# Performance work log

Hardware: AMD Instinct MI355X
Metric: run time of the kernel (lower is better)

## Reference

```python
import jax, jax.numpy as jnp
import numpy as np

ALPHA = 0.2
NEG_INF = -9e15


def setup_inputs() -> dict:
    key = jax.random.key(0)
    k1, k2, k3, k4 = jax.random.split(key, 4)
    B, N, C_IN, C_OUT, R, H = 8, 1024, 256, 256, 4, 4
    node_feats = jax.random.normal(k1, (B, N, C_IN), dtype=jnp.float32)
    adj_matrix = jax.random.randint(k2, (B, N, N, R), 0, 2, dtype=jnp.int32)
    # xavier_uniform with gain=1.414 for Linear(c_in, c_out) weights
    lim_w = 1.414 * np.sqrt(6.0 / (C_IN + C_OUT))
    W = jax.random.uniform(k3, (R, C_IN, C_OUT), minval=-lim_w, maxval=lim_w, dtype=jnp.float32)
    c_per = C_OUT // H
    lim_a = 1.414 * np.sqrt(6.0 / (H + 2 * c_per))
    a = jax.random.uniform(k4, (R, H, 2 * c_per), minval=-lim_a, maxval=lim_a, dtype=jnp.float32)
    return {"node_feats": node_feats, "adj_matrix": adj_matrix, "W": W, "a": a}


def reference(node_feats, adj_matrix, W, a):
    B, N, _ = node_feats.shape
    R, H = a.shape[0], a.shape[1]
    C = a.shape[2] // 2  # per-head feature dim
    out = jnp.zeros((B, N, H, C), dtype=node_feats.dtype)
    for r in range(R):
        # per-relation projection: [B,N,H,C]
        f = jnp.einsum('bnc,cd->bnd', node_feats, W[r]).reshape(B, N, H, C)
        a_l, a_r = a[r, :, :C], a[r, :, C:]
        # attention logit decomposes: a . [f_i || f_j] = a_l . f_i + a_r . f_j
        li = jnp.einsum('bnhc,hc->bnh', f, a_l)  # source-node term
        lj = jnp.einsum('bnhc,hc->bnh', f, a_r)  # target-node term
        logits = jax.nn.leaky_relu(li[:, :, None, :] + lj[:, None, :, :], ALPHA)  # [B,N,N,H]
        mask = adj_matrix[..., r] != 0  # [B,N,N]
        logits = jnp.where(mask[..., None], logits, NEG_INF)
        probs = jax.nn.softmax(logits, axis=2)
        out = out + jnp.einsum('bijh,bjhc->bihc', probs, f)
    # concat_heads=True
    return out.reshape(B, N, H * C)
```

## Files before the change

kernel.cpp:

```cpp
#include <hip/hip_runtime.h>
#include <math.h>

#define Bsz 8
#define Nn 1024
#define CIN 256
#define COUT 256
#define NR 4
#define NH 4

typedef unsigned short u16;
typedef __attribute__((ext_vector_type(8))) short bf16x8;
typedef __attribute__((ext_vector_type(4))) float f32x4;

#define OFF_LIP (16u << 20)
#define OFF_LJP ((16u << 20) + (512u << 10))
#define OFF_ADJM (17u << 20)
#define OFF_XBF (21u << 20)
#define OFF_WBFT (25u << 20)
#define OFF_WAL ((25u << 20) + (512u << 10))
#define OFF_WAR ((25u << 20) + (528u << 10))

#define LOG2E 1.4426950408889634f

__device__ __forceinline__ short f2bf(float x) {
  union { float f; unsigned u; } v; v.f = x;
  unsigned r = (v.u + 0x7FFFu + ((v.u >> 16) & 1u)) >> 16;
  return (short)r;
}

__device__ __forceinline__ float fast_exp2(float x) {
#if __has_builtin(__builtin_amdgcn_exp2f)
  return __builtin_amdgcn_exp2f(x);
#else
  return exp2f(x);
#endif
}

__device__ __forceinline__ void gl_lds16(const void* g, void* l) {
  __builtin_amdgcn_global_load_lds(
      (const __attribute__((address_space(1))) unsigned int*)(unsigned long long)g,
      (__attribute__((address_space(3))) unsigned int*)(unsigned int)(unsigned long long)l,
      16, 0, 0);
}

__global__ __launch_bounds__(256, 8)
void gatt_pack(const int4* __restrict__ adj4, unsigned long long* __restrict__ adjm) {
  const int t = threadIdx.x;
  const int wid = blockIdx.x * 4 + (t >> 6);
  const int lane = t & 63;
  const int jw = wid & 15;
  const int i = (wid >> 4) & 1023;
  const int b = wid >> 14;
  const int j = jw * 64 + lane;
  const int4 av = adj4[(size_t)(b * Nn + i) * Nn + j];
  const unsigned long long b0 = __ballot(av.x != 0);
  const unsigned long long b1 = __ballot(av.y != 0);
  const unsigned long long b2 = __ballot(av.z != 0);
  const unsigned long long b3 = __ballot(av.w != 0);
  if (lane < 4) {
    unsigned long long v = (lane == 0) ? b0 : (lane == 1) ? b1 : (lane == 2) ? b2 : b3;
    adjm[((size_t)((b * Nn + i) * NR + lane)) * 16 + jw] = v;
  }
}

__global__ __launch_bounds__(256, 8)
void gatt_xconv(const float4* __restrict__ X4, int4* __restrict__ Xbf4) {
  const int idx = blockIdx.x * 256 + threadIdx.x;
  const float4 a = X4[idx * 2], b = X4[idx * 2 + 1];
  u16 pk[8];
  pk[0] = (u16)f2bf(a.x); pk[1] = (u16)f2bf(a.y); pk[2] = (u16)f2bf(a.z); pk[3] = (u16)f2bf(a.w);
  pk[4] = (u16)f2bf(b.x); pk[5] = (u16)f2bf(b.y); pk[6] = (u16)f2bf(b.z); pk[7] = (u16)f2bf(b.w);
  Xbf4[idx] = *(int4*)pk;
}

__global__ __launch_bounds__(256, 4)
void gatt_wtrans(const float* __restrict__ W, u16* __restrict__ WbfT) {
  const int t = threadIdx.x;
  const int r = blockIdx.x >> 3, kc = blockIdx.x & 7;
  u16 pk[32];
#pragma unroll 8
  for (int kk = 0; kk < 32; ++kk)
    pk[kk] = (u16)f2bf(W[(size_t)r * 65536 + (size_t)(kc * 32 + kk) * COUT + t]);
  u16* dst = WbfT + (size_t)r * 65536 + (size_t)t * CIN + kc * 32;
#pragma unroll
  for (int q = 0; q < 4; ++q) *(int4*)(dst + q * 8) = *(int4*)(pk + q * 8);
}

__global__ __launch_bounds__(256, 4)
void gatt_wa(const float* __restrict__ W, const float* __restrict__ a,
             float* __restrict__ wa_l, float* __restrict__ wa_r) {
  const int t = threadIdx.x;
  const int r = blockIdx.x >> 2, h = blockIdx.x & 3;
  float sl = 0.f, sr = 0.f;
  const float* Wp = W + (size_t)r * 65536 + (size_t)t * COUT + h * 64;
  const float* ap = a + r * 512 + h * 128;
#pragma unroll 8
  for (int c = 0; c < 64; ++c) {
    const float wv = Wp[c];
    sl = fmaf(wv, ap[c], sl);
    sr = fmaf(wv, ap[64 + c], sr);
  }
  wa_l[(size_t)blockIdx.x * CIN + t] = sl;
  wa_r[(size_t)blockIdx.x * CIN + t] = sr;
}

__global__ __launch_bounds__(256, 4)
void gatt_logit(const float* __restrict__ X, const float4* __restrict__ wal4,
                const float4* __restrict__ war4, float* __restrict__ Lip,
                float* __restrict__ Ljp) {
  __shared__ float Xs[16 * 260];
  const int t = threadIdx.x;
  const int row0 = blockIdx.x * 16;
  {
    const int il = t >> 4, kq = t & 15;
    const float4* xp = (const float4*)(X + (size_t)(row0 + il) * CIN + kq * 16);
    float4* dst = (float4*)(Xs + il * 260 + kq * 16);
#pragma unroll
    for (int u = 0; u < 4; ++u) dst[u] = xp[u];
  }
  __syncthreads();
  const int rl = t >> 4, combo = t & 15;
  float li = 0.f, lj = 0.f;
#pragma unroll 8
  for (int k4 = 0; k4 < 64; ++k4) {
    const float4 x4 = *(const float4*)(Xs + rl * 260 + k4 * 4);
    const float4 wl = wal4[combo * 64 + k4];
    const float4 wr = war4[combo * 64 + k4];
    li += x4.x * wl.x + x4.y * wl.y + x4.z * wl.z + x4.w * wl.w;
    lj += x4.x * wr.x + x4.y * wr.y + x4.z * wr.z + x4.w * wr.w;
  }
  const int g = row0 + rl, b = g >> 10, n = g & 1023;
  const size_t idx = ((size_t)(combo * Bsz + b)) * Nn + n;
  Lip[idx] = li * LOG2E;
  Ljp[idx] = lj * LOG2E;
}

__global__ __launch_bounds__(256)
void gatt_fgemm(const u16* __restrict__ Xbf, const u16* __restrict__ WbfT,
                u16* __restrict__ fTf) {
  __shared__ u16 lds_w[8192];
  __shared__ u16 lds_x[2048];
  const int t = threadIdx.x;
  const int r = blockIdx.x & 3, b = (blockIdx.x >> 2) & 7, ntl = blockIdx.x >> 5;
  const int n0 = ntl * 64;
  const int g0 = b * Nn + n0;
  const int lane = t & 63, w = t >> 6;
  const int m = lane & 15, quad = lane >> 4;
  const int cw = w * 64;
  const int xq = quad ^ (m & 3);

  const u16* Wsrc = WbfT + (size_t)r * 65536;
  f32x4 acc[4][4];
#pragma unroll
  for (int ct = 0; ct < 4; ++ct)
#pragma unroll
    for (int nt = 0; nt < 4; ++nt) acc[ct][nt] = (f32x4){0.f, 0.f, 0.f, 0.f};

  for (int kc = 0; kc < 8; ++kc) {
    __syncthreads();
#pragma unroll
    for (int q = 0; q < 4; ++q) {
      const int s = q * 256 + t;
      const int c = s >> 2, ks = (s & 3) ^ (c & 3);
      gl_lds16(Wsrc + (size_t)c * CIN + kc * 32 + ks * 8, lds_w + s * 8);
    }
    {
      const int s = t;
      const int n = s >> 2, ks = (s & 3) ^ (n & 3);
      gl_lds16(Xbf + (size_t)(g0 + n) * CIN + kc * 32 + ks * 8, lds_x + s * 8);
    }
    __syncthreads();

    bf16x8 af[4], bfr[4];
#pragma unroll
    for (int ct = 0; ct < 4; ++ct)
      af[ct] = *(const bf16x8*)(lds_w + (cw + ct * 16 + m) * 32 + xq * 8);
#pragma unroll
    for (int nt = 0; nt < 4; ++nt)
      bfr[nt] = *(const bf16x8*)(lds_x + (nt * 16 + m) * 32 + xq * 8);
#pragma unroll
    for (int ct = 0; ct < 4; ++ct)
#pragma unroll
      for (int nt = 0; nt < 4; ++nt)
        acc[ct][nt] = __builtin_amdgcn_mfma_f32_16x16x32_bf16(af[ct], bfr[nt], acc[ct][nt], 0, 0, 0);
  }

  u16* fragbase = fTf + (size_t)(((r * Bsz + b) * 4 + w) * 128) * 512;
#pragma unroll
  for (int ct = 0; ct < 4; ++ct) {
#pragma unroll
    for (int ntf = 0; ntf < 4; ++ntf) {
      const int j = n0 + ntf * 16 + m;
      const int jb = j >> 5;
      const int qt = ((ntf & 1) << 1) | (m >> 3);
      const int e = m & 7;
      u16* dst = fragbase + (size_t)((jb * 4 + ct) * 512) + (qt * 16 + quad * 4) * 8 + e;
#pragma unroll
      for (int p = 0; p < 4; ++p) dst[p * 8] = (u16)f2bf(acc[ct][ntf][p]);
    }
  }
}

__global__ __launch_bounds__(256, 4)
void gatt_attn(const unsigned long long* __restrict__ adjm,
               const u16* __restrict__ fTf, const float* __restrict__ Lip,
               const float* __restrict__ Ljp, float* __restrict__ out) {
  __shared__ float ljs[4 * 1024];

  const int t = threadIdx.x;
  const int comb = blockIdx.x & 31;
  const int b = comb >> 2, r = comb & 3;
  const int i0 = (blockIdx.x >> 5) * 32;
  const int h = t >> 6, lane = t & 63;
  const int m = lane & 15, quad = lane >> 4;
  const int qo = quad * 8;

  {
#pragma unroll
    for (int q = 0; q < 4; ++q) {
      const int s = q * 256 + t;
      const int hh = s >> 8, off = s & 255;
      ((float4*)ljs)[hh * 256 + off] =
          ((const float4*)(Ljp + ((size_t)((r * NH + hh) * Bsz + b)) * Nn))[off];
    }
  }
  __syncthreads();

  const float* lipb = Lip + ((size_t)((r * NH + h) * Bsz + b)) * Nn;
  const float li0 = lipb[i0 + m];
  const float li1 = lipb[i0 + 16 + m];
  const unsigned long long* amp0 = adjm + ((size_t)((b * Nn + i0 + m) * NR + r)) * 16;
  const unsigned long long* amp1 = adjm + ((size_t)((b * Nn + i0 + 16 + m) * NR + r)) * 16;
  const bf16x8* fp = (const bf16x8*)fTf + (size_t)(((r * Bsz + b) * 4 + h)) * 8192;
  const float* ljh = ljs + h * Nn;

  bf16x8 ones;
#pragma unroll
  for (int e = 0; e < 8; ++e) ones[e] = (short)0x3F80;

  f32x4 acc[2][4], den[2];
#pragma unroll
  for (int iw = 0; iw < 2; ++iw) {
    den[iw] = (f32x4){0.f, 0.f, 0.f, 0.f};
#pragma unroll
    for (int nt = 0; nt < 4; ++nt) acc[iw][nt] = (f32x4){0.f, 0.f, 0.f, 0.f};
  }

  for (int jq = 0; jq < 16; ++jq) {
    const uint2 mw0 = *(const uint2*)(amp0 + jq);
    const uint2 mw1 = *(const uint2*)(amp1 + jq);
#pragma unroll
    for (int half = 0; half < 2; ++half) {
      const int jb = jq * 2 + half;
      const unsigned mb0 = ((half ? mw0.y : mw0.x) >> qo) & 0xFFu;
      const unsigned mb1 = ((half ? mw1.y : mw1.x) >> qo) & 0xFFu;
      const float4 la = *(const float4*)(ljh + jb * 32 + qo);
      const float4 lb = *(const float4*)(ljh + jb * 32 + qo + 4);
      const float ljv[8] = {la.x, la.y, la.z, la.w, lb.x, lb.y, lb.z, lb.w};
      bf16x8 bfr[4];
#pragma unroll
      for (int nt = 0; nt < 4; ++nt) bfr[nt] = fp[(jb * 4 + nt) * 64 + lane];
#pragma unroll
      for (int iw = 0; iw < 2; ++iw) {
        const float liv = iw ? li1 : li0;
        const unsigned mb = iw ? mb1 : mb0;
        unsigned wm[8];
#pragma unroll
        for (int e = 0; e < 8; ++e) {
          const float s = liv + ljv[e];
          const float ls = fmaxf(s, 0.2f * s);
          const float wv = fast_exp2(ls);
          const int msk = ((int)(mb << (31 - e))) >> 31;
          wm[e] = __float_as_uint(wv) & (unsigned)msk;
        }
        union { unsigned u[4]; bf16x8 v; } af;
#pragma unroll
        for (int k = 0; k < 4; ++k)
          af.u[k] = (wm[2 * k] >> 16) | (wm[2 * k + 1] & 0xFFFF0000u);
        den[iw] = __builtin_amdgcn_mfma_f32_16x16x32_bf16(af.v, ones, den[iw], 0, 0, 0);
#pragma unroll
        for (int nt = 0; nt < 4; ++nt)
          acc[iw][nt] = __builtin_amdgcn_mfma_f32_16x16x32_bf16(af.v, bfr[nt], acc[iw][nt], 0, 0, 0);
      }
    }
  }

#pragma unroll
  for (int iw = 0; iw < 2; ++iw) {
#pragma unroll
    for (int p = 0; p < 4; ++p) {
      const float inv = __builtin_amdgcn_rcpf(den[iw][p]);
      const int i = i0 + iw * 16 + quad * 4 + p;
      float* op = out + ((size_t)(b * Nn) + i) * COUT + h * 64 + m;
#pragma unroll
      for (int nt = 0; nt < 4; ++nt) atomicAdd(op + nt * 16, acc[iw][nt][p] * inv);
    }
  }
}

extern "C" void kernel_launch(void* const* d_in, const int* in_sizes, int n_in,
                              void* d_out, int out_size, void* d_ws, size_t ws_size,
                              hipStream_t stream) {
  const float* X = (const float*)d_in[0];
  const int4* adj4 = (const int4*)d_in[1];
  const float* W = (const float*)d_in[2];
  const float* a = (const float*)d_in[3];
  float* out = (float*)d_out;

  char* ws = (char*)d_ws;
  u16* fTf = (u16*)ws;
  float* Lip = (float*)(ws + OFF_LIP);
  float* Ljp = (float*)(ws + OFF_LJP);
  unsigned long long* adjm = (unsigned long long*)(ws + OFF_ADJM);
  u16* Xbf = (u16*)(ws + OFF_XBF);
  u16* WbfT = (u16*)(ws + OFF_WBFT);
  float* wa_l = (float*)(ws + OFF_WAL);
  float* wa_r = (float*)(ws + OFF_WAR);

  hipMemsetAsync(d_out, 0, (size_t)out_size * sizeof(float), stream);
  gatt_pack<<<dim3(32768), dim3(256), 0, stream>>>(adj4, adjm);
  gatt_xconv<<<dim3(1024), dim3(256), 0, stream>>>((const float4*)X, (int4*)Xbf);
  gatt_wtrans<<<dim3(32), dim3(256), 0, stream>>>(W, WbfT);
  gatt_wa<<<dim3(16), dim3(256), 0, stream>>>(W, a, wa_l, wa_r);
  gatt_logit<<<dim3(512), dim3(256), 0, stream>>>(X, (const float4*)wa_l,
                                                  (const float4*)wa_r, Lip, Ljp);
  gatt_fgemm<<<dim3(512), dim3(256), 0, stream>>>(Xbf, WbfT, fTf);
  gatt_attn<<<dim3(1024), dim3(256), 0, stream>>>(adjm, fTf, Lip, Ljp, out);
}
```

Measured before the change: 309.0 us.

## Merge prep kernels, fuse X conversion into logits, replace atomics with reduce

Merges the W transpose and W·a kernels into one launch, and converts X to bf16 inside the logit kernel so the separate conversion kernel goes away. The attention kernel now writes per-relation partial outputs to workspace with plain stores, and a new reduce kernel sums the four relations. This replaces the memset and the float atomics. The attention inner loop also switches to packed float2 math, sbfe mask extraction and perm-based bf16 packing to cut ALU work. In exchange it adds a 32 MB workspace round-trip for the partial outputs.

```diff
diff --git a/kernel.cpp b/kernel.cpp
--- a/kernel.cpp
+++ b/kernel.cpp
@@ -11,6 +11,7 @@
 typedef unsigned short u16;
 typedef __attribute__((ext_vector_type(8))) short bf16x8;
 typedef __attribute__((ext_vector_type(4))) float f32x4;
+typedef __attribute__((ext_vector_type(2))) float f32x2;
 
 #define OFF_LIP (16u << 20)
 #define OFF_LJP ((16u << 20) + (512u << 10))
@@ -19,6 +20,7 @@
 #define OFF_WBFT (25u << 20)
 #define OFF_WAL ((25u << 20) + (512u << 10))
 #define OFF_WAR ((25u << 20) + (528u << 10))
+#define OFF_OUTR (26u << 20)
 
 #define LOG2E 1.4426950408889634f
 
@@ -33,6 +35,22 @@
   return __builtin_amdgcn_exp2f(x);
 #else
   return exp2f(x);
+#endif
+}
+
+__device__ __forceinline__ int sbfe1(unsigned v, int bit) {
+#if __has_builtin(__builtin_amdgcn_sbfe)
+  return __builtin_amdgcn_sbfe((int)v, bit, 1);
+#else
+  return ((int)(v << (31 - bit))) >> 31;
+#endif
+}
+
+__device__ __forceinline__ unsigned perm_hi16(unsigned hi, unsigned lo) {
+#if __has_builtin(__builtin_amdgcn_perm)
+  return __builtin_amdgcn_perm(hi, lo, 0x07060302u);
+#else
+  return (lo >> 16) | (hi & 0xFFFF0000u);
 #endif
 }
 
@@ -63,60 +81,63 @@
   }
 }
 
-__global__ __launch_bounds__(256, 8)
-void gatt_xconv(const float4* __restrict__ X4, int4* __restrict__ Xbf4) {
-  const int idx = blockIdx.x * 256 + threadIdx.x;
-  const float4 a = X4[idx * 2], b = X4[idx * 2 + 1];
-  u16 pk[8];
-  pk[0] = (u16)f2bf(a.x); pk[1] = (u16)f2bf(a.y); pk[2] = (u16)f2bf(a.z); pk[3] = (u16)f2bf(a.w);
-  pk[4] = (u16)f2bf(b.x); pk[5] = (u16)f2bf(b.y); pk[6] = (u16)f2bf(b.z); pk[7] = (u16)f2bf(b.w);
-  Xbf4[idx] = *(int4*)pk;
-}
-
 __global__ __launch_bounds__(256, 4)
-void gatt_wtrans(const float* __restrict__ W, u16* __restrict__ WbfT) {
-  const int t = threadIdx.x;
-  const int r = blockIdx.x >> 3, kc = blockIdx.x & 7;
-  u16 pk[32];
+void gatt_prep(const float* __restrict__ W, const float* __restrict__ a,
+               u16* __restrict__ WbfT, float* __restrict__ wa_l,
+               float* __restrict__ wa_r) {
+  const int t = threadIdx.x;
+  if (blockIdx.x < 32) {
+    const int r = blockIdx.x >> 3, kc = blockIdx.x & 7;
+    u16 pk[32];
 #pragma unroll 8
-  for (int kk = 0; kk < 32; ++kk)
-    pk[kk] = (u16)f2bf(W[(size_t)r * 65536 + (size_t)(kc * 32 + kk) * COUT + t]);
-  u16* dst = WbfT + (size_t)r * 65536 + (size_t)t * CIN + kc * 32;
-#pragma unroll
-  for (int q = 0; q < 4; ++q) *(int4*)(dst + q * 8) = *(int4*)(pk + q * 8);
+    for (int kk = 0; kk < 32; ++kk)
+      pk[kk] = (u16)f2bf(W[(size_t)r * 65536 + (size_t)(kc * 32 + kk) * COUT + t]);
+    u16* dst = WbfT + (size_t)r * 65536 + (size_t)t * CIN + kc * 32;
+#pragma unroll
+    for (int q = 0; q < 4; ++q) *(int4*)(dst + q * 8) = *(int4*)(pk + q * 8);
+  } else {
+    const int cb = blockIdx.x - 32;
+    const int r = cb >> 2, h = cb & 3;
+    float sl = 0.f, sr = 0.f;
+    const float* Wp = W + (size_t)r * 65536 + (size_t)t * COUT + h * 64;
+    const float* ap = a + r * 512 + h * 128;
+#pragma unroll 8
+    for (int c = 0; c < 64; ++c) {
+      const float wv = Wp[c];
+      sl = fmaf(wv, ap[c], sl);
+      sr = fmaf(wv, ap[64 + c], sr);
+    }
+    wa_l[(size_t)cb * CIN + t] = sl;
+    wa_r[(size_t)cb * CIN + t] = sr;
+  }
 }
 
 __global__ __launch_bounds__(256, 4)
-void gatt_wa(const float* __restrict__ W, const float* __restrict__ a,
-             float* __restrict__ wa_l, float* __restrict__ wa_r) {
-  const int t = threadIdx.x;
-  const int r = blockIdx.x >> 2, h = blockIdx.x & 3;
-  float sl = 0.f, sr = 0.f;
-  const float* Wp = W + (size_t)r * 65536 + (size_t)t * COUT + h * 64;
-  const float* ap = a + r * 512 + h * 128;
-#pragma unroll 8
-  for (int c = 0; c < 64; ++c) {
-    const float wv = Wp[c];
-    sl = fmaf(wv, ap[c], sl);
-    sr = fmaf(wv, ap[64 + c], sr);
-  }
-  wa_l[(size_t)blockIdx.x * CIN + t] = sl;
-  wa_r[(size_t)blockIdx.x * CIN + t] = sr;
-}
-
-__global__ __launch_bounds__(256, 4)
-void gatt_logit(const float* __restrict__ X, const float4* __restrict__ wal4,
-                const float4* __restrict__ war4, float* __restrict__ Lip,
-                float* __restrict__ Ljp) {
+void gatt_logitx(const float* __restrict__ X, const float4* __restrict__ wal4,
+                 const float4* __restrict__ war4, float* __restrict__ Lip,
+                 float* __restrict__ Ljp, u16* __restrict__ Xbf) {
   __shared__ float Xs[16 * 260];
   const int t = threadIdx.x;
   const int row0 = blockIdx.x * 16;
   {
     const int il = t >> 4, kq = t & 15;
     const float4* xp = (const float4*)(X + (size_t)(row0 + il) * CIN + kq * 16);
+    float4 v[4];
+    u16 pk[16];
+#pragma unroll
+    for (int u = 0; u < 4; ++u) {
+      v[u] = xp[u];
+      pk[u * 4 + 0] = (u16)f2bf(v[u].x);
+      pk[u * 4 + 1] = (u16)f2bf(v[u].y);
+      pk[u * 4 + 2] = (u16)f2bf(v[u].z);
+      pk[u * 4 + 3] = (u16)f2bf(v[u].w);
+    }
     float4* dst = (float4*)(Xs + il * 260 + kq * 16);
 #pragma unroll
-    for (int u = 0; u < 4; ++u) dst[u] = xp[u];
+    for (int u = 0; u < 4; ++u) dst[u] = v[u];
+    u16* xb = Xbf + (size_t)(row0 + il) * CIN + kq * 16;
+    *(int4*)xb = *(int4*)pk;
+    *(int4*)(xb + 8) = *(int4*)(pk + 8);
   }
   __syncthreads();
   const int rl = t >> 4, combo = t & 15;
@@ -204,7 +225,7 @@
 __global__ __launch_bounds__(256, 4)
 void gatt_attn(const unsigned long long* __restrict__ adjm,
                const u16* __restrict__ fTf, const float* __restrict__ Lip,
-               const float* __restrict__ Ljp, float* __restrict__ out) {
+               const float* __restrict__ Ljp, float* __restrict__ outr) {
   __shared__ float ljs[4 * 1024];
 
   const int t = threadIdx.x;
@@ -252,31 +273,32 @@
 #pragma unroll
     for (int half = 0; half < 2; ++half) {
       const int jb = jq * 2 + half;
-      const unsigned mb0 = ((half ? mw0.y : mw0.x) >> qo) & 0xFFu;
-      const unsigned mb1 = ((half ? mw1.y : mw1.x) >> qo) & 0xFFu;
-      const float4 la = *(const float4*)(ljh + jb * 32 + qo);
-      const float4 lb = *(const float4*)(ljh + jb * 32 + qo + 4);
-      const float ljv[8] = {la.x, la.y, la.z, la.w, lb.x, lb.y, lb.z, lb.w};
+      const unsigned w0 = half ? mw0.y : mw0.x;
+      const unsigned w1 = half ? mw1.y : mw1.x;
+      const f32x2* lj2p = (const f32x2*)(ljh + jb * 32 + qo);
       bf16x8 bfr[4];
 #pragma unroll
       for (int nt = 0; nt < 4; ++nt) bfr[nt] = fp[(jb * 4 + nt) * 64 + lane];
 #pragma unroll
       for (int iw = 0; iw < 2; ++iw) {
         const float liv = iw ? li1 : li0;
-        const unsigned mb = iw ? mb1 : mb0;
-        unsigned wm[8];
-#pragma unroll
-        for (int e = 0; e < 8; ++e) {
-          const float s = liv + ljv[e];
-          const float ls = fmaxf(s, 0.2f * s);
-          const float wv = fast_exp2(ls);
-          const int msk = ((int)(mb << (31 - e))) >> 31;
-          wm[e] = __float_as_uint(wv) & (unsigned)msk;
+        const unsigned mb = (iw ? w1 : w0) >> qo;
+        const f32x2 li2 = {liv, liv};
+        unsigned afu[4];
+#pragma unroll
+        for (int pr = 0; pr < 4; ++pr) {
+          const f32x2 s2 = li2 + lj2p[pr];
+          const f32x2 s02 = s2 * 0.2f;
+          const float t0 = fmaxf(s2.x, s02.x);
+          const float t1 = fmaxf(s2.y, s02.y);
+          const unsigned e0 =
+              __float_as_uint(fast_exp2(t0)) & (unsigned)sbfe1(mb, 2 * pr);
+          const unsigned e1 =
+              __float_as_uint(fast_exp2(t1)) & (unsigned)sbfe1(mb, 2 * pr + 1);
+          afu[pr] = perm_hi16(e1, e0);
         }
         union { unsigned u[4]; bf16x8 v; } af;
-#pragma unroll
-        for (int k = 0; k < 4; ++k)
-          af.u[k] = (wm[2 * k] >> 16) | (wm[2 * k + 1] & 0xFFFF0000u);
+        af.u[0] = afu[0]; af.u[1] = afu[1]; af.u[2] = afu[2]; af.u[3] = afu[3];
         den[iw] = __builtin_amdgcn_mfma_f32_16x16x32_bf16(af.v, ones, den[iw], 0, 0, 0);
 #pragma unroll
         for (int nt = 0; nt < 4; ++nt)
@@ -291,11 +313,22 @@
     for (int p = 0; p < 4; ++p) {
       const float inv = __builtin_amdgcn_rcpf(den[iw][p]);
       const int i = i0 + iw * 16 + quad * 4 + p;
-      float* op = out + ((size_t)(b * Nn) + i) * COUT + h * 64 + m;
-#pragma unroll
-      for (int nt = 0; nt < 4; ++nt) atomicAdd(op + nt * 16, acc[iw][nt][p] * inv);
-    }
-  }
+      float* op = outr + (((size_t)(r * Bsz + b) * Nn) + i) * COUT + h * 64 + m;
+#pragma unroll
+      for (int nt = 0; nt < 4; ++nt) op[nt * 16] = acc[iw][nt][p] * inv;
+    }
+  }
+}
+
+__global__ __launch_bounds__(256, 8)
+void gatt_reduce(const float4* __restrict__ outr4, float4* __restrict__ out4) {
+  const int idx = blockIdx.x * 256 + threadIdx.x;
+  float4 v0 = outr4[idx];
+  float4 v1 = outr4[idx + 524288];
+  float4 v2 = outr4[idx + 2 * 524288];
+  float4 v3 = outr4[idx + 3 * 524288];
+  out4[idx] = make_float4(v0.x + v1.x + v2.x + v3.x, v0.y + v1.y + v2.y + v3.y,
+                          v0.z + v1.z + v2.z + v3.z, v0.w + v1.w + v2.w + v3.w);
 }
 
 extern "C" void kernel_launch(void* const* d_in, const int* in_sizes, int n_in,
@@ -316,14 +349,13 @@
   u16* WbfT = (u16*)(ws + OFF_WBFT);
   float* wa_l = (float*)(ws + OFF_WAL);
   float* wa_r = (float*)(ws + OFF_WAR);
-
-  hipMemsetAsync(d_out, 0, (size_t)out_size * sizeof(float), stream);
+  float* outr = (float*)(ws + OFF_OUTR);
+
   gatt_pack<<<dim3(32768), dim3(256), 0, stream>>>(adj4, adjm);
-  gatt_xconv<<<dim3(1024), dim3(256), 0, stream>>>((const float4*)X, (int4*)Xbf);
-  gatt_wtrans<<<dim3(32), dim3(256), 0, stream>>>(W, WbfT);
-  gatt_wa<<<dim3(16), dim3(256), 0, stream>>>(W, a, wa_l, wa_r);
-  gatt_logit<<<dim3(512), dim3(256), 0, stream>>>(X, (const float4*)wa_l,
-                                                  (const float4*)wa_r, Lip, Ljp);
+  gatt_prep<<<dim3(48), dim3(256), 0, stream>>>(W, a, WbfT, wa_l, wa_r);
+  gatt_logitx<<<dim3(512), dim3(256), 0, stream>>>(X, (const float4*)wa_l,
+                                                   (const float4*)wa_r, Lip, Ljp, Xbf);
   gatt_fgemm<<<dim3(512), dim3(256), 0, stream>>>(Xbf, WbfT, fTf);
-  gatt_attn<<<dim3(1024), dim3(256), 0, stream>>>(adjm, fTf, Lip, Ljp, out);
-}
+  gatt_attn<<<dim3(1024), dim3(256), 0, stream>>>(adjm, fTf, Lip, Ljp, outr);
+  gatt_reduce<<<dim3(2048), dim3(256), 0, stream>>>((const float4*)outr, (float4*)out);
+}
```

New measurement: 294.7 us. -4.6%, faster.
